# Kernel tuning notes

Measured on AMD Instinct MI355X. Metric: run time of the kernel, lower is better.

The kernel has to match this reference:

```python
import jax, jax.numpy as jnp
import numpy as np

B, S, D, H = 2, 2048, 1024, 16
HD = D // H


def setup_inputs() -> dict:
    key = jax.random.key(0)
    ks = jax.random.split(key, 9)
    sc = 0.02
    return {
        "x": jax.random.normal(ks[0], (B, S, D), dtype=jnp.float32),
        "qw": jax.random.normal(ks[1], (D, D), dtype=jnp.float32) * sc,
        "qb": jax.random.normal(ks[2], (D,), dtype=jnp.float32) * sc,
        "kw": jax.random.normal(ks[3], (D, D), dtype=jnp.float32) * sc,
        "kb": jax.random.normal(ks[4], (D,), dtype=jnp.float32) * sc,
        "vw": jax.random.normal(ks[5], (D, D), dtype=jnp.float32) * sc,
        "vb": jax.random.normal(ks[6], (D,), dtype=jnp.float32) * sc,
        "ow": jax.random.normal(ks[7], (D, D), dtype=jnp.float32) * sc,
        "ob": jax.random.normal(ks[8], (D,), dtype=jnp.float32) * sc,
    }


def reference(x, qw, qb, kw, kb, vw, vb, ow, ob):
    b, s, d = x.shape
    # projections (torch Linear: x @ W.T + b)
    q = (x @ qw.T + qb).reshape(b, s, H, HD).transpose(0, 2, 1, 3)  # bhsd
    k = (x @ kw.T + kb).reshape(b, s, H, HD).transpose(0, 2, 1, 3)
    v = (x @ vw.T + vb).reshape(b, s, H, HD).transpose(0, 2, 1, 3)
    scale = 1.0 / jnp.sqrt(jnp.float32(HD))
    score = jnp.einsum("bhsd,bhtd->bhst", q, k) * scale  # bhss
    # causal mask: -inf strictly above diagonal
    mask = jnp.triu(jnp.full((s, s), -jnp.inf, dtype=score.dtype), k=1)
    score = jax.nn.softmax(score + mask, axis=-1)
    o = jnp.einsum("bhst,bhtd->bhsd", score, v)
    o = o.transpose(0, 2, 1, 3).reshape(b, s, d)
    return o @ ow.T + ob
```

## Files before the change

### kernel.cpp

```cpp
#include <hip/hip_runtime.h>
#include <hip/hip_bf16.h>
#include <stdint.h>

typedef __bf16 bf16x8 __attribute__((ext_vector_type(8)));
typedef __bf16 bf16x4 __attribute__((ext_vector_type(4)));
typedef float f32x4 __attribute__((ext_vector_type(4)));
typedef unsigned short ushort_t;


__device__ inline ushort_t f2bf(float f) {
  union { float f; uint32_t u; } v; v.f = f;
  uint32_t r = (v.u + 0x7fffu + ((v.u >> 16) & 1u)) >> 16;
  return (ushort_t)r;
}

__device__ inline void gll16(const void* g, void* l) {
  __builtin_amdgcn_global_load_lds((const __attribute__((address_space(1))) void*)g,
                                   (__attribute__((address_space(3))) void*)l, 16, 0, 0);
}

__global__ void cvt_all(const float* __restrict__ x,
                        const float* __restrict__ qw, const float* __restrict__ kw,
                        const float* __restrict__ vw, const float* __restrict__ ow,
                        ushort_t* __restrict__ xb, ushort_t* __restrict__ wb) {
  int bid = blockIdx.x;
  const float* s;
  ushort_t* o;
  int i;
  if (bid < 4096) {
    s = x; o = xb; i = bid * 256 + threadIdx.x;
  } else {
    int j = bid - 4096;
    int wi = j >> 10;
    const float* srcs[4] = {qw, kw, vw, ow};
    s = srcs[wi];
    o = wb + (size_t)wi * 1048576;
    i = (j & 1023) * 256 + threadIdx.x;
  }
  float4 f = ((const float4*)s)[i];
  union { ushort_t u[4]; uint2 v; } r;
  r.u[0] = f2bf(f.x); r.u[1] = f2bf(f.y); r.u[2] = f2bf(f.z); r.u[3] = f2bf(f.w);
  ((uint2*)o)[i] = r.v;
}

#define NKT 16

__device__ inline void stage_half(const ushort_t* __restrict__ g, ushort_t* l, int tid) {
  #pragma unroll
  for (int i = 0; i < 2; i++) {
    int c = tid + i * 512;
    int row = c >> 3;
    int q = (c & 7) ^ (row & 7);
    gll16(g + (size_t)row * 1024 + q * 8, l + c * 8);
  }
}

__global__ __launch_bounds__(512, 2) void qkv_gemm(
    const ushort_t* __restrict__ xb,
    const ushort_t* __restrict__ qwb, const ushort_t* __restrict__ kwb, const ushort_t* __restrict__ vwb,
    const float* __restrict__ qbias, const float* __restrict__ kbias, const float* __restrict__ vbias,
    ushort_t* __restrict__ qo, ushort_t* __restrict__ ko, ushort_t* __restrict__ vto)
{
  const int z = blockIdx.y;
  const int bx = blockIdx.x;
  const float* bias = (z == 0) ? qbias : (z == 1) ? kbias : vbias;
  const ushort_t* Ap;
  const ushort_t* Bp;
  int m0, n0;
  if (z == 2) {
    Ap = vwb; Bp = xb;
    m0 = (bx & 3) * 256;
    n0 = (bx >> 2) * 256;
  } else {
    Ap = xb; Bp = (z == 0) ? qwb : kwb;
    m0 = (bx >> 2) * 256;
    n0 = (bx & 3) * 256;
  }

  __shared__ __align__(16) ushort_t As[2][2][128 * 64];
  __shared__ __align__(16) ushort_t Bs[2][2][128 * 64];

  const int tid = threadIdx.x;
  const int w = tid >> 6;
  const int lane = tid & 63;
  const int ln = lane & 15;
  const int q4 = lane >> 4;
  const int wm = w & 1;
  const int wn = w >> 1;
  const int bh = wn >> 1;
  const int brow0 = (wn & 1) * 64;

  f32x4 acc[8][4];
  #pragma unroll
  for (int i = 0; i < 8; i++)
    #pragma unroll
    for (int j = 0; j < 4; j++) acc[i][j] = f32x4{0.f, 0.f, 0.f, 0.f};

  stage_half(Ap + (size_t)(m0 +   0) * 1024 +  0, &As[0][0][0], tid);
  stage_half(Ap + (size_t)(m0 + 128) * 1024 +  0, &As[0][1][0], tid);
  stage_half(Bp + (size_t)(n0 +   0) * 1024 +  0, &Bs[0][0][0], tid);
  stage_half(Bp + (size_t)(n0 + 128) * 1024 +  0, &Bs[0][1][0], tid);
  stage_half(Bp + (size_t)(n0 +   0) * 1024 + 64, &Bs[1][0][0], tid);
  stage_half(Bp + (size_t)(n0 + 128) * 1024 + 64, &Bs[1][1][0], tid);
  asm volatile("s_waitcnt vmcnt(4)" ::: "memory");
  __builtin_amdgcn_s_barrier();

  const int achk = ln & 7;

  for (int t = 0; t < NKT; ++t) {
    const int buf = t & 1;
    const ushort_t* Abuf = &As[buf][wm][0];
    const ushort_t* Bbuf = &Bs[buf][bh][0];

    bf16x8 a0[4][2], a4[4][2], b0[2][2], b2[2][2];

    #pragma unroll
    for (int m = 0; m < 4; m++)
      #pragma unroll
      for (int ks = 0; ks < 2; ks++)
        a0[m][ks] = *(const bf16x8*)&Abuf[(m * 16 + ln) * 64 + (((ks * 4 + q4) ^ achk) * 8)];
    #pragma unroll
    for (int n = 0; n < 2; n++)
      #pragma unroll
      for (int ks = 0; ks < 2; ks++)
        b0[n][ks] = *(const bf16x8*)&Bbuf[(brow0 + n * 16 + ln) * 64 + (((ks * 4 + q4) ^ achk) * 8)];
    if (t + 1 < NKT)
      stage_half(Ap + (size_t)m0 * 1024 + (t + 1) * 64, &As[(t + 1) & 1][0][0], tid);
    __builtin_amdgcn_s_barrier();
    asm volatile("s_waitcnt lgkmcnt(0)" ::: "memory");
    __builtin_amdgcn_s_setprio(1);
    #pragma unroll
    for (int m = 0; m < 4; m++)
      #pragma unroll
      for (int n = 0; n < 2; n++)
        #pragma unroll
        for (int ks = 0; ks < 2; ks++)
          acc[m][n] = __builtin_amdgcn_mfma_f32_16x16x32_bf16(a0[m][ks], b0[n][ks], acc[m][n], 0, 0, 0);
    __builtin_amdgcn_s_setprio(0);
    __builtin_amdgcn_s_barrier();

    #pragma unroll
    for (int n = 0; n < 2; n++)
      #pragma unroll
      for (int ks = 0; ks < 2; ks++)
        b2[n][ks] = *(const bf16x8*)&Bbuf[(brow0 + (n + 2) * 16 + ln) * 64 + (((ks * 4 + q4) ^ achk) * 8)];
    if (t + 1 < NKT)
      stage_half(Ap + (size_t)(m0 + 128) * 1024 + (t + 1) * 64, &As[(t + 1) & 1][1][0], tid);
    __builtin_amdgcn_s_barrier();
    asm volatile("s_waitcnt lgkmcnt(0)" ::: "memory");
    __builtin_amdgcn_s_setprio(1);
    #pragma unroll
    for (int m = 0; m < 4; m++)
      #pragma unroll
      for (int n = 0; n < 2; n++)
        #pragma unroll
        for (int ks = 0; ks < 2; ks++)
          acc[m][n + 2] = __builtin_amdgcn_mfma_f32_16x16x32_bf16(a0[m][ks], b2[n][ks], acc[m][n + 2], 0, 0, 0);
    __builtin_amdgcn_s_setprio(0);
    __builtin_amdgcn_s_barrier();

    #pragma unroll
    for (int m = 0; m < 4; m++)
      #pragma unroll
      for (int ks = 0; ks < 2; ks++)
        a4[m][ks] = *(const bf16x8*)&Abuf[((m + 4) * 16 + ln) * 64 + (((ks * 4 + q4) ^ achk) * 8)];
    if (t + 2 < NKT)
      stage_half(Bp + (size_t)n0 * 1024 + (t + 2) * 64, &Bs[buf][0][0], tid);
    __builtin_amdgcn_s_barrier();
    asm volatile("s_waitcnt lgkmcnt(0)" ::: "memory");
    __builtin_amdgcn_s_setprio(1);
    #pragma unroll
    for (int m = 0; m < 4; m++)
      #pragma unroll
      for (int n = 0; n < 2; n++)
        #pragma unroll
        for (int ks = 0; ks < 2; ks++)
          acc[m + 4][n + 2] = __builtin_amdgcn_mfma_f32_16x16x32_bf16(a4[m][ks], b2[n][ks], acc[m + 4][n + 2], 0, 0, 0);
    __builtin_amdgcn_s_setprio(0);
    __builtin_amdgcn_s_barrier();

    if (t + 2 < NKT)
      stage_half(Bp + (size_t)(n0 + 128) * 1024 + (t + 2) * 64, &Bs[buf][1][0], tid);
    __builtin_amdgcn_s_barrier();
    __builtin_amdgcn_s_setprio(1);
    #pragma unroll
    for (int m = 0; m < 4; m++)
      #pragma unroll
      for (int n = 0; n < 2; n++)
        #pragma unroll
        for (int ks = 0; ks < 2; ks++)
          acc[m + 4][n] = __builtin_amdgcn_mfma_f32_16x16x32_bf16(a4[m][ks], b0[n][ks], acc[m + 4][n], 0, 0, 0);
    __builtin_amdgcn_s_setprio(0);
    if (t + 2 < NKT) {
      asm volatile("s_waitcnt vmcnt(4)" ::: "memory");
    } else if (t + 1 < NKT) {
      asm volatile("s_waitcnt vmcnt(0)" ::: "memory");
    }
    __builtin_amdgcn_s_barrier();
  }

  if (z == 2) {
    #pragma unroll
    for (int n = 0; n < 4; n++) {
      int col = n0 + wn * 64 + n * 16 + ln;
      int bb = col >> 11, s = col & 2047;
      size_t base = (size_t)bb * 2097152 + s;
      #pragma unroll
      for (int m = 0; m < 8; m++) {
        int prow = m0 + wm * 128 + m * 16 + q4 * 4;
        #pragma unroll
        for (int r = 0; r < 4; r++) {
          int p = prow + r;
          vto[base + (size_t)p * 2048] = f2bf(acc[m][n][r] + bias[p]);
        }
      }
    }
  } else {
    #pragma unroll
    for (int n = 0; n < 4; n++) {
      int col = n0 + wn * 64 + n * 16 + ln;
      float bv = bias[col];
      int h = col >> 6, hd = col & 63;
      #pragma unroll
      for (int m = 0; m < 8; m++) {
        int rowb = m0 + wm * 128 + m * 16 + q4 * 4;
        #pragma unroll
        for (int r = 0; r < 4; r++) {
          int row = rowb + r;
          int b = row >> 11, s = row & 2047;
          float val = acc[m][n][r] + bv;
          if (z == 0) {
            qo[((size_t)((b * 16 + h) * 2048 + s)) * 64 + hd] = f2bf(val * 0.180336884f);
          } else {
            ko[((size_t)((b * 16 + h) * 2048 + s)) * 64 + hd] = f2bf(val);
          }
        }
      }
    }
  }
}

#define PAD 72
#define PPAD 68
__global__ __launch_bounds__(512) void attn(
    const ushort_t* __restrict__ qp, const ushort_t* __restrict__ kp,
    const ushort_t* __restrict__ vtp, ushort_t* __restrict__ op)
{
  __shared__ __align__(16) ushort_t Ks[2][64 * PAD];
  __shared__ __align__(16) ushort_t Vts[2][64 * PAD];
  __shared__ __align__(16) ushort_t Ps[8][16 * PPAD];

  const int tid = threadIdx.x;
  const int w = tid >> 6;
  const int lane = tid & 63;
  const int ln = lane & 15;
  const int q4 = lane >> 4;
  const int bh = blockIdx.y;
  const int b = bh >> 4, h = bh & 15;
  int tswz = (blockIdx.x + blockIdx.y) & 15;
  const int qt = (blockIdx.y & 16) ? (15 - tswz) : tswz;
  const int q0 = qt * 128;
  const int nt = 2 * qt + 2;

  const int kr_row = tid >> 3, kr_col = (tid & 7) * 8;

  bf16x8 onesf;
  {
    union { ushort_t u[8]; bf16x8 v; } t;
    #pragma unroll
    for (int j = 0; j < 8; j++) t.u[j] = 0x3F80;
    onesf = t.v;
  }

  bf16x8 qf[2];
  {
    const ushort_t* base = qp + ((size_t)bh * 2048 + q0 + w * 16 + ln) * 64 + q4 * 8;
    qf[0] = *(const bf16x8*)(base);
    qf[1] = *(const bf16x8*)(base + 32);
  }

  f32x4 acc_o[4];
  f32x4 acc_l = f32x4{0.f, 0.f, 0.f, 0.f};
  #pragma unroll
  for (int t = 0; t < 4; t++) acc_o[t] = f32x4{0.f, 0.f, 0.f, 0.f};

  const ushort_t* kb = kp + (size_t)bh * 2048 * 64;
  const ushort_t* vb = vtp + (size_t)bh * 64 * 2048;

  uint4 kr, vr;
  kr = *(const uint4*)(kb + kr_row * 64 + kr_col);
  vr = *(const uint4*)(vb + (size_t)kr_row * 2048 + kr_col);
  *(uint4*)(&Ks [0][kr_row * PAD + kr_col]) = kr;
  *(uint4*)(&Vts[0][kr_row * PAD + kr_col]) = vr;
  kr = *(const uint4*)(kb + 64 * 64 + kr_row * 64 + kr_col);
  vr = *(const uint4*)(vb + (size_t)kr_row * 2048 + 64 + kr_col);

  for (int it = 0; it < nt; it++) {
    const int cur = it & 1;
    __syncthreads();
    if (it + 1 < nt) {
      const int nxt = cur ^ 1;
      *(uint4*)(&Ks [nxt][kr_row * PAD + kr_col]) = kr;
      *(uint4*)(&Vts[nxt][kr_row * PAD + kr_col]) = vr;
    }
    if (it + 2 < nt) {
      int kv2 = (it + 2) * 64;
      kr = *(const uint4*)(kb + (size_t)kv2 * 64 + kr_row * 64 + kr_col);
      vr = *(const uint4*)(vb + (size_t)kr_row * 2048 + kv2 + kr_col);
    }

    f32x4 sc[4];
    #pragma unroll
    for (int t = 0; t < 4; t++) sc[t] = f32x4{0.f, 0.f, 0.f, 0.f};
    __builtin_amdgcn_s_setprio(1);
    #pragma unroll
    for (int ks = 0; ks < 2; ks++) {
      bf16x8 kf[4];
      #pragma unroll
      for (int tn = 0; tn < 4; tn++)
        kf[tn] = *(const bf16x8*)(&Ks[cur][(tn * 16 + ln) * PAD + ks * 32 + q4 * 8]);
      #pragma unroll
      for (int tn = 0; tn < 4; tn++)
        sc[tn] = __builtin_amdgcn_mfma_f32_16x16x32_bf16(qf[ks], kf[tn], sc[tn], 0, 0, 0);
    }
    __builtin_amdgcn_s_setprio(0);

    if (it >= 2 * qt) {
      int qrow = q0 + w * 16 + q4 * 4;
      int kv0 = it * 64;
      #pragma unroll
      for (int tn = 0; tn < 4; tn++) {
        int col = kv0 + tn * 16 + ln;
        #pragma unroll
        for (int r = 0; r < 4; r++)
          if (col > qrow + r) sc[tn][r] = -__builtin_inff();
      }
    }
    #pragma unroll
    for (int tn = 0; tn < 4; tn++)
      #pragma unroll
      for (int r = 0; r < 4; r++) {
        float p = __builtin_amdgcn_exp2f(sc[tn][r]);
        Ps[w][(q4 * 4 + r) * PPAD + tn * 16 + ln] = (ushort_t)(__float_as_uint(p) >> 16);
      }
    __builtin_amdgcn_s_setprio(1);
    #pragma unroll
    for (int ks = 0; ks < 2; ks++) {
      bf16x8 vf[4];
      #pragma unroll
      for (int tn = 0; tn < 4; tn++)
        vf[tn] = *(const bf16x8*)(&Vts[cur][(tn * 16 + ln) * PAD + ks * 32 + q4 * 8]);
      const ushort_t* pp = &Ps[w][ln * PPAD + ks * 32 + q4 * 8];
      bf16x4 plo = *(const bf16x4*)(pp);
      bf16x4 phi = *(const bf16x4*)(pp + 4);
      bf16x8 pf = __builtin_shufflevector(plo, phi, 0, 1, 2, 3, 4, 5, 6, 7);
      acc_l = __builtin_amdgcn_mfma_f32_16x16x32_bf16(pf, onesf, acc_l, 0, 0, 0);
      #pragma unroll
      for (int tn = 0; tn < 4; tn++)
        acc_o[tn] = __builtin_amdgcn_mfma_f32_16x16x32_bf16(pf, vf[tn], acc_o[tn], 0, 0, 0);
    }
    __builtin_amdgcn_s_setprio(0);
  }

  {
    float invl[4];
    #pragma unroll
    for (int r = 0; r < 4; r++) invl[r] = __builtin_amdgcn_rcpf(acc_l[r]);
    #pragma unroll
    for (int tn = 0; tn < 4; tn++)
      #pragma unroll
      for (int r = 0; r < 4; r++) {
        int row = q0 + w * 16 + q4 * 4 + r;
        op[((size_t)b * 2048 + row) * 1024 + h * 64 + tn * 16 + ln] =
            f2bf(acc_o[tn][r] * invl[r]);
      }
  }
}

__global__ __launch_bounds__(256) void out_gemm(
    const ushort_t* __restrict__ ob_in, const ushort_t* __restrict__ owb,
    const float* __restrict__ obias, float* __restrict__ out)
{
  __shared__ __align__(16) ushort_t As[3][64 * 64];
  __shared__ __align__(16) ushort_t Bs[3][128 * 64];

  const int tid = threadIdx.x;
  const int w = tid >> 6;
  const int lane = tid & 63;
  const int ln = lane & 15;
  const int q4 = lane >> 4;
  const int wm = w & 1, wn = w >> 1;
  const int m0 = blockIdx.y * 64;
  const int n0 = blockIdx.x * 128;

  f32x4 acc[2][4];
  #pragma unroll
  for (int i = 0; i < 2; i++)
    #pragma unroll
    for (int j = 0; j < 4; j++) acc[i][j] = f32x4{0.f, 0.f, 0.f, 0.f};

  auto STAGE = [&](int bi, int k0) {
    #pragma unroll
    for (int i = 0; i < 2; i++) {
      int c = tid + i * 256;
      int row = c >> 3;
      int cq = (c & 7) ^ (row & 7);
      gll16(&ob_in[(size_t)(m0 + row) * 1024 + k0 + cq * 8], &As[bi][c * 8]);
    }
    #pragma unroll
    for (int i = 0; i < 4; i++) {
      int c = tid + i * 256;
      int row = c >> 3;
      int cq = (c & 7) ^ (row & 7);
      gll16(&owb[(size_t)(n0 + row) * 1024 + k0 + cq * 8], &Bs[bi][c * 8]);
    }
  };

  STAGE(0, 0);
  STAGE(1, 64);
  asm volatile("s_waitcnt vmcnt(6)" ::: "memory");
  __builtin_amdgcn_s_barrier();

  #pragma unroll
  for (int t = 0; t < 16; t++) {
    const int cb = t % 3;
    if (t + 2 < 16) STAGE((t + 2) % 3, (t + 2) * 64);
    #pragma unroll
    for (int ks = 0; ks < 2; ks++) {
      bf16x8 af[2], bfr[4];
      #pragma unroll
      for (int tt = 0; tt < 2; tt++) {
        int rr = wm * 32 + tt * 16 + ln;
        af[tt] = *(const bf16x8*)(&As[cb][rr * 64 + (((ks * 4 + q4) ^ (rr & 7)) * 8)]);
      }
      #pragma unroll
      for (int tt = 0; tt < 4; tt++) {
        int rc = wn * 64 + tt * 16 + ln;
        bfr[tt] = *(const bf16x8*)(&Bs[cb][rc * 64 + (((ks * 4 + q4) ^ (rc & 7)) * 8)]);
      }
      #pragma unroll
      for (int tm = 0; tm < 2; tm++)
        #pragma unroll
        for (int tn = 0; tn < 4; tn++)
          acc[tm][tn] = __builtin_amdgcn_mfma_f32_16x16x32_bf16(af[tm], bfr[tn], acc[tm][tn], 0, 0, 0);
    }
    if (t + 2 < 16) {
      asm volatile("s_waitcnt vmcnt(6)" ::: "memory");
    } else if (t + 1 < 16) {
      asm volatile("s_waitcnt vmcnt(0)" ::: "memory");
    }
    __builtin_amdgcn_s_barrier();
  }

  #pragma unroll
  for (int tn = 0; tn < 4; tn++) {
    int col = n0 + wn * 64 + tn * 16 + ln;
    float bv = obias[col];
    #pragma unroll
    for (int tm = 0; tm < 2; tm++) {
      int rowb = m0 + wm * 32 + tm * 16 + q4 * 4;
      #pragma unroll
      for (int r = 0; r < 4; r++)
        out[(size_t)(rowb + r) * 1024 + col] = acc[tm][tn][r] + bv;
    }
  }
}

extern "C" void kernel_launch(void* const* d_in, const int* in_sizes, int n_in,
                              void* d_out, int out_size, void* d_ws, size_t ws_size,
                              hipStream_t stream) {
  const float* x     = (const float*)d_in[0];
  const float* qw    = (const float*)d_in[1];
  const float* qb    = (const float*)d_in[2];
  const float* kw    = (const float*)d_in[3];
  const float* kb    = (const float*)d_in[4];
  const float* vw    = (const float*)d_in[5];
  const float* vb    = (const float*)d_in[6];
  const float* ow    = (const float*)d_in[7];
  const float* obias = (const float*)d_in[8];
  float* out = (float*)d_out;

  char* ws = (char*)d_ws;
  ushort_t* xb  = (ushort_t*)(ws);
  ushort_t* wb  = (ushort_t*)(ws + 8388608);
  ushort_t* qwb = wb;
  ushort_t* kwb = wb + 1048576;
  ushort_t* vwb = wb + 2097152;
  ushort_t* owb = wb + 3145728;
  ushort_t* qo  = (ushort_t*)(ws + 16777216);
  ushort_t* ko  = (ushort_t*)(ws + 25165824);
  ushort_t* vto = (ushort_t*)(ws + 33554432);
  ushort_t* oo  = (ushort_t*)(ws + 41943040);

  cvt_all<<<dim3(8192), dim3(256), 0, stream>>>(x, qw, kw, vw, ow, xb, wb);

  qkv_gemm<<<dim3(64, 3), dim3(512), 0, stream>>>(xb, qwb, kwb, vwb, qb, kb, vb, qo, ko, vto);
  attn<<<dim3(16, 32), dim3(512), 0, stream>>>(qo, ko, vto, oo);
  out_gemm<<<dim3(8, 64), dim3(256), 0, stream>>>(oo, owb, obias, out);
}
```

Before: 180.5 us.

## Load K/V tiles via direct global-to-LDS with XOR swizzle in attention

Replaces the register-staged K and V tile prefetch (global load into registers, then LDS store) with global_load_lds 16-byte direct transfers into double-buffered LDS. The padded LDS layout is replaced by an unpadded 64-wide layout with an XOR chunk swizzle to avoid bank conflicts on fragment reads. Synchronization moves to a vmcnt wait plus barrier at the end of each iteration. This saves VGPRs and LDS store instructions, but it shortens the prefetch distance from two tiles to one and waits on all outstanding loads every iteration.

```diff
diff --git a/kernel.cpp b/kernel.cpp
--- a/kernel.cpp
+++ b/kernel.cpp
@@ -240,14 +240,13 @@
   }
 }
 
-#define PAD 72
 #define PPAD 68
 __global__ __launch_bounds__(512) void attn(
     const ushort_t* __restrict__ qp, const ushort_t* __restrict__ kp,
     const ushort_t* __restrict__ vtp, ushort_t* __restrict__ op)
 {
-  __shared__ __align__(16) ushort_t Ks[2][64 * PAD];
-  __shared__ __align__(16) ushort_t Vts[2][64 * PAD];
+  __shared__ __align__(16) ushort_t Ks[2][64 * 64];
+  __shared__ __align__(16) ushort_t Vts[2][64 * 64];
   __shared__ __align__(16) ushort_t Ps[8][16 * PPAD];
 
   const int tid = threadIdx.x;
@@ -262,7 +261,8 @@
   const int q0 = qt * 128;
   const int nt = 2 * qt + 2;
 
-  const int kr_row = tid >> 3, kr_col = (tid & 7) * 8;
+  const int sr_row = tid >> 3;
+  const int sr_q = (tid & 7) ^ (sr_row & 7);
 
   bf16x8 onesf;
   {
@@ -287,26 +287,19 @@
   const ushort_t* kb = kp + (size_t)bh * 2048 * 64;
   const ushort_t* vb = vtp + (size_t)bh * 64 * 2048;
 
-  uint4 kr, vr;
-  kr = *(const uint4*)(kb + kr_row * 64 + kr_col);
-  vr = *(const uint4*)(vb + (size_t)kr_row * 2048 + kr_col);
-  *(uint4*)(&Ks [0][kr_row * PAD + kr_col]) = kr;
-  *(uint4*)(&Vts[0][kr_row * PAD + kr_col]) = vr;
-  kr = *(const uint4*)(kb + 64 * 64 + kr_row * 64 + kr_col);
-  vr = *(const uint4*)(vb + (size_t)kr_row * 2048 + 64 + kr_col);
+  gll16(kb + (size_t)sr_row * 64 + sr_q * 8, &Ks[0][tid * 8]);
+  gll16(vb + (size_t)sr_row * 2048 + sr_q * 8, &Vts[0][tid * 8]);
+  asm volatile("s_waitcnt vmcnt(0)" ::: "memory");
+  __builtin_amdgcn_s_barrier();
+
+  const int fchk = ln & 7;
 
   for (int it = 0; it < nt; it++) {
     const int cur = it & 1;
-    __syncthreads();
     if (it + 1 < nt) {
-      const int nxt = cur ^ 1;
-      *(uint4*)(&Ks [nxt][kr_row * PAD + kr_col]) = kr;
-      *(uint4*)(&Vts[nxt][kr_row * PAD + kr_col]) = vr;
-    }
-    if (it + 2 < nt) {
-      int kv2 = (it + 2) * 64;
-      kr = *(const uint4*)(kb + (size_t)kv2 * 64 + kr_row * 64 + kr_col);
-      vr = *(const uint4*)(vb + (size_t)kr_row * 2048 + kv2 + kr_col);
+      int kv1 = (it + 1) * 64;
+      gll16(kb + (size_t)(kv1 + sr_row) * 64 + sr_q * 8, &Ks[cur ^ 1][tid * 8]);
+      gll16(vb + (size_t)sr_row * 2048 + kv1 + sr_q * 8, &Vts[cur ^ 1][tid * 8]);
     }
 
     f32x4 sc[4];
@@ -318,7 +311,7 @@
       bf16x8 kf[4];
       #pragma unroll
       for (int tn = 0; tn < 4; tn++)
-        kf[tn] = *(const bf16x8*)(&Ks[cur][(tn * 16 + ln) * PAD + ks * 32 + q4 * 8]);
+        kf[tn] = *(const bf16x8*)(&Ks[cur][(tn * 16 + ln) * 64 + (((ks * 4 + q4) ^ fchk) * 8)]);
       #pragma unroll
       for (int tn = 0; tn < 4; tn++)
         sc[tn] = __builtin_amdgcn_mfma_f32_16x16x32_bf16(qf[ks], kf[tn], sc[tn], 0, 0, 0);
@@ -349,7 +342,7 @@
       bf16x8 vf[4];
       #pragma unroll
       for (int tn = 0; tn < 4; tn++)
-        vf[tn] = *(const bf16x8*)(&Vts[cur][(tn * 16 + ln) * PAD + ks * 32 + q4 * 8]);
+        vf[tn] = *(const bf16x8*)(&Vts[cur][(tn * 16 + ln) * 64 + (((ks * 4 + q4) ^ fchk) * 8)]);
       const ushort_t* pp = &Ps[w][ln * PPAD + ks * 32 + q4 * 8];
       bf16x4 plo = *(const bf16x4*)(pp);
       bf16x4 phi = *(const bf16x4*)(pp + 4);
@@ -360,6 +353,11 @@
         acc_o[tn] = __builtin_amdgcn_mfma_f32_16x16x32_bf16(pf, vf[tn], acc_o[tn], 0, 0, 0);
     }
     __builtin_amdgcn_s_setprio(0);
+
+    if (it + 1 < nt) {
+      asm volatile("s_waitcnt vmcnt(0)" ::: "memory");
+      __builtin_amdgcn_s_barrier();
+    }
   }
 
   {
```

After: 186.4 us. +3.3%, slower.
